# Kernel tuning notes

Measured on AMD Instinct MI355X. Metric: run time of the kernel, lower is better.

Reference implementation:

```python
import jax, jax.numpy as jnp
import numpy as np

NUMV = 779
B, NQ, NV = 1, 65536, 1558


def feat_sample(feat, xy):
    # feat [B,C,H,W], xy [B,N,2] in [-1,1]; bilinear, align_corners=True (grid_sample semantics)
    Bn, C, H, W = feat.shape
    x = (xy[..., 0] + 1.0) * 0.5 * (W - 1)
    y = (xy[..., 1] + 1.0) * 0.5 * (H - 1)
    x0f = jnp.floor(x); y0f = jnp.floor(y)
    wx = (x - x0f)[:, None, :]; wy = (y - y0f)[:, None, :]  # [B,1,N]
    x0 = jnp.clip(x0f, 0, W - 1).astype(jnp.int32)
    x1 = jnp.clip(x0f + 1, 0, W - 1).astype(jnp.int32)
    y0 = jnp.clip(y0f, 0, H - 1).astype(jnp.int32)
    y1 = jnp.clip(y0f + 1, 0, H - 1).astype(jnp.int32)
    g = jax.vmap(lambda f, yi, xi: f[:, yi, xi])  # [C,N] per batch
    v00 = g(feat, y0, x0); v01 = g(feat, y0, x1)
    v10 = g(feat, y1, x0); v11 = g(feat, y1, x1)
    out = v00 * (1 - wx) * (1 - wy) + v01 * wx * (1 - wy) + v10 * (1 - wx) * wy + v11 * wx * wy
    return jnp.transpose(out, (0, 2, 1))  # [B,N,C]


def conv2d(x, w):
    return jax.lax.conv_general_dilated(x, w, (1, 1), ((1, 1), (1, 1)), dimension_numbers=('NCHW', 'OIHW', 'NCHW'))


def conv1d3(x, w):
    return jax.lax.conv_general_dilated(x, w, (1,), ((1, 1),), dimension_numbers=('NCH', 'OIH', 'NCH'))


def ln(x, g, b):
    # LayerNorm over trailing dims matching g's shape, eps=1e-6
    axes = tuple(range(x.ndim - g.ndim, x.ndim))
    m = x.mean(axes, keepdims=True)
    v = x.var(axes, keepdims=True)
    return (x - m) / jnp.sqrt(v + 1e-6) * g + b


def apool3(x):
    # AdaptiveAvgPool2d(3), PyTorch window rule: [floor(i*L/3), ceil((i+1)*L/3))
    H, W = x.shape[-2], x.shape[-1]
    bnd = lambda L: [(int(np.floor(i * L / 3)), int(np.ceil((i + 1) * L / 3))) for i in range(3)]
    hb, wb = bnd(H), bnd(W)
    rows = []
    for (hs, he) in hb:
        rows.append(jnp.stack([x[:, :, hs:he, ws:we].mean((-2, -1)) for (ws, we) in wb], axis=-1))
    return jnp.stack(rows, axis=-2)  # [B,C,3,3]


def _forward(vert_xy, ft1, ft_xy, vert, v, vert_vis, query_vis, img_xy, img_fmap, latent_fused, fconv_w1, fconv_w2, at_w1, at_w2, gt_w1, gt_g1, gt_b1, gt_w2, gt_g2, gt_b2, c3_w1, c3_g1, c3_b1, c3_w2, c3_g2, c3_b2, c4_w1, c4_g1, c4_b1, c4_w2, c4_g2, c4_b2):
    Bn = vert_xy.shape[0]
    vf = jnp.concatenate([feat_sample(img_fmap, vert_xy), feat_sample(ft1, vert_xy)], axis=2)  # [B,NV,11]
    h = jax.nn.relu(ln(conv2d(ft1, c3_w1), c3_g1, c3_b1))
    h = jax.nn.relu(ln(conv2d(h, c3_w2), c3_g2, c3_b2))
    gf = apool3(h).reshape(Bn, 42, 9)
    h = jax.nn.relu(ln(conv2d(img_fmap, c4_w1), c4_g1, c4_b1))
    h = jax.nn.relu(ln(conv2d(h, c4_w2), c4_g2, c4_b2))
    gf_img = apool3(h).reshape(Bn, 42, 9)
    gf = jnp.concatenate([gf_img, gf], axis=-1)  # [B,42,18]
    h = jax.nn.relu(ln(conv1d3(gf, gt_w1), gt_g1, gt_b1))
    gf_vert = jax.nn.relu(ln(conv1d3(h, gt_w2), gt_g2, gt_b2))  # [B,1558,18]
    vf = jnp.concatenate([vf, gf_vert], axis=2)  # [B,1558,29]
    # KNN, K=1; indices taken from batch 0 exactly as the original does
    d2 = (v[0] ** 2).sum(-1)[:, None] + (vert[0] ** 2).sum(-1)[None, :] - 2.0 * jnp.einsum('qd,pd->qp', v[0], vert[0])  # [NQ,NV]
    idx = jnp.argmin(d2, axis=-1)  # [NQ]
    vf_toh = jnp.concatenate([vf[:, NUMV:], vf[:, :NUMV]], axis=1)
    vv_toh = jnp.concatenate([vert_vis[:, NUMV:], vert_vis[:, :NUMV]], axis=1)
    knn = vf[:, idx] * vert_vis[:, idx]        # [B,NQ,29]
    knn_toh = vf_toh[:, idx] * vv_toh[:, idx]
    vis_th = vert_vis[:, idx]                  # [B,NQ,1]
    vis_toh = vv_toh[:, idx]
    knn_gf, knn_f = knn[:, :, 11:], knn[:, :, :11]
    knn_toh_gf, knn_toh_f = knn_toh[:, :, 11:], knn_toh[:, :, :11]
    query_feat = jnp.concatenate([img_xy, ft_xy], axis=2)  # [B,NQ,11]
    y = jnp.concatenate([query_feat, knn_f, knn_toh_f, knn_gf, knn_toh_gf, latent_fused, query_vis, vis_th, vis_toh], axis=2)  # [B,NQ,96]
    at = jax.nn.sigmoid(jnp.einsum('oc,bnc->bno', at_w2, jax.nn.relu(jnp.einsum('oc,bnc->bno', at_w1, y))))  # [B,NQ,6]
    y2 = jnp.concatenate([query_feat * at[..., 0:1], knn_f * at[..., 1:2], knn_toh_f * at[..., 2:3], knn_gf * at[..., 3:4], knn_toh_gf * at[..., 4:5], latent_fused * at[..., 5:6], query_vis, vis_th, vis_toh], axis=2)  # [B,NQ,96]
    return jnp.einsum('oc,bnc->bno', fconv_w2, jax.nn.relu(jnp.einsum('oc,bnc->bno', fconv_w1, y2)))  # [B,NQ,40]


def setup_inputs():
    key = jax.random.key(0)
    ks = jax.random.split(key, 24)
    rn = lambda k, s, sc=1.0: jax.random.normal(k, s, dtype=jnp.float32) * sc
    return {
        'vert_xy': jax.random.uniform(ks[0], (B, NV, 2), minval=-1.0, maxval=1.0),
        'ft1': rn(ks[1], (B, 8, 64, 64)),
        'ft_xy': rn(ks[2], (B, NQ, 8)),
        'vert': rn(ks[3], (B, NV, 3)),
        'v': rn(ks[4], (B, NQ, 3)),
        'vert_vis': jax.random.uniform(ks[5], (B, NV, 1)),
        'query_vis': jax.random.uniform(ks[6], (B, NQ, 1)),
        'img_xy': rn(ks[7], (B, NQ, 3)),
        'img_fmap': rn(ks[8], (B, 3, 256, 256)),
        'latent_fused': rn(ks[9], (B, NQ, 24)),
        'fconv_w1': rn(ks[10], (96, 96), 0.1), 'fconv_w2': rn(ks[11], (40, 96), 0.1),
        'at_w1': rn(ks[12], (96, 96), 0.1), 'at_w2': rn(ks[13], (6, 96), 0.1),
        'gt_w1': rn(ks[14], (NUMV, 42, 3), 0.05), 'gt_g1': jnp.ones(18), 'gt_b1': jnp.zeros(18),
        'gt_w2': rn(ks[15], (2 * NUMV, NUMV, 3), 0.02), 'gt_g2': jnp.ones(18), 'gt_b2': jnp.zeros(18),
        'c3_w1': rn(ks[16], (21, 8, 3, 3), 0.1), 'c3_g1': jnp.ones((64, 64)), 'c3_b1': jnp.zeros((64, 64)),
        'c3_w2': rn(ks[17], (42, 21, 3, 3), 0.1), 'c3_g2': jnp.ones((64, 64)), 'c3_b2': jnp.zeros((64, 64)),
        'c4_w1': rn(ks[18], (21, 3, 3, 3), 0.1), 'c4_g1': jnp.ones((256, 256)), 'c4_b1': jnp.zeros((256, 256)),
        'c4_w2': rn(ks[19], (42, 21, 3, 3), 0.1), 'c4_g2': jnp.ones((256, 256)), 'c4_b2': jnp.zeros((256, 256)),
    }


def reference(vert_xy, ft1, ft_xy, vert, v, vert_vis, query_vis, img_xy, img_fmap, latent_fused, fconv_w1, fconv_w2, at_w1, at_w2, gt_w1, gt_g1, gt_b1, gt_w2, gt_g2, gt_b2, c3_w1, c3_g1, c3_b1, c3_w2, c3_g2, c3_b2, c4_w1, c4_g1, c4_b1, c4_w2, c4_g2, c4_b2):
    return _forward(vert_xy, ft1, ft_xy, vert, v, vert_vis, query_vis, img_xy, img_fmap, latent_fused, fconv_w1, fconv_w2, at_w1, at_w2, gt_w1, gt_g1, gt_b1, gt_w2, gt_g2, gt_b2, c3_w1, c3_g1, c3_b1, c3_w2, c3_g2, c3_b2, c4_w1, c4_g1, c4_b1, c4_w2, c4_g2, c4_b2)
```

## Files before the change

kernel.cpp:

```cpp
#include <hip/hip_runtime.h>
#include <hip/hip_bf16.h>
#include <math.h>

#define NQ_    65536
#define NV_    1558
#define HALF_V 779
#define VSPLIT 8
#define VCHUNK 195

#define WS_STATS 0
#define WS_GFC   512
#define WS_GTH   1280
#define WS_VF    15360
#define WS_C3A   65536
#define WS_C3B   151552
#define WS_C4A   323584
#define WS_C4B   1699840
#define WS_WBF   4452352
#define WS_PART  4464640
#define WS_IDX   4500480
#define WS_BESTD 4566016
#define WS_BESTI 5090304
#define WS_VERT4 5614592

typedef __attribute__((ext_vector_type(8))) short bf16x8;
typedef __attribute__((ext_vector_type(4))) float f32x4;

__device__ __forceinline__ short f2b(float x) {
    union { __hip_bfloat16 h; short s; } u; u.h = __float2bfloat16(x); return u.s;
}

__device__ __forceinline__ void bsample(const float* __restrict__ f, int C, int H, int W,
                                        float xn, float yn, float* __restrict__ o) {
    float x = (xn + 1.f) * 0.5f * (float)(W - 1);
    float y = (yn + 1.f) * 0.5f * (float)(H - 1);
    float x0f = floorf(x), y0f = floorf(y);
    float wx = x - x0f, wy = y - y0f;
    int x0 = (int)fminf(fmaxf(x0f, 0.f), (float)(W - 1));
    int x1 = (int)fminf(fmaxf(x0f + 1.f, 0.f), (float)(W - 1));
    int y0 = (int)fminf(fmaxf(y0f, 0.f), (float)(H - 1));
    int y1 = (int)fminf(fmaxf(y0f + 1.f, 0.f), (float)(H - 1));
    for (int c = 0; c < C; ++c) {
        const float* b = f + c * H * W;
        float v00 = b[y0 * W + x0], v01 = b[y0 * W + x1];
        float v10 = b[y1 * W + x0], v11 = b[y1 * W + x1];
        o[c] = v00 * (1.f - wx) * (1.f - wy) + v01 * wx * (1.f - wy)
             + v10 * (1.f - wx) * wy       + v11 * wx * wy;
    }
}

__device__ __forceinline__ void feat_body(int rb, int tid,
                                          const float* __restrict__ vert_xy,
                                          const float* __restrict__ img,
                                          const float* __restrict__ ft1,
                                          float* __restrict__ vf) {
    int v = rb * 256 + tid;
    if (v >= NV_) return;
    float xn = vert_xy[v * 2 + 0], yn = vert_xy[v * 2 + 1];
    float tmp[8];
    bsample(img, 3, 256, 256, xn, yn, tmp);
    float* o = vf + v * 32;
    o[0] = tmp[0]; o[1] = tmp[1]; o[2] = tmp[2];
    bsample(ft1, 8, 64, 64, xn, yn, tmp);
    #pragma unroll
    for (int c = 0; c < 8; ++c) o[3 + c] = tmp[c];
}

template <int CB>
__device__ __forceinline__ void conv_body(
    float* __restrict__ sm, int tid,
    const float* __restrict__ in, const float* __restrict__ w,
    float* __restrict__ out, float* __restrict__ part,
    int Cin, int H, int W, int bx, int by, int nbx) {
    int c0 = by * CB;
    int gpx0 = bx * 1024;
    int y0 = gpx0 / W;
    int tileF = 1024 + 2 * W;
    int nf4 = tileF >> 2;
    int HW = H * W;
    int px0 = tid * 4;
    int ty = px0 / W, x = px0 % W;

    float acc[CB][4];
    #pragma unroll
    for (int j = 0; j < CB; ++j)
        #pragma unroll
        for (int p = 0; p < 4; ++p) acc[j][p] = 0.f;

    const float* wbase = w + c0 * Cin * 9;
    float4 sreg[2];

    #pragma unroll
    for (int k = 0; k < 2; ++k) {
        int idx = tid + k * 256;
        float4 v = make_float4(0.f, 0.f, 0.f, 0.f);
        if (idx < nf4) {
            int gw = idx * 4;
            int gy = y0 - 1 + gw / W, gx = gw % W;
            if (gy >= 0 && gy < H) v = *(const float4*)(in + gy * W + gx);
        }
        sreg[k] = v;
    }
    #pragma unroll
    for (int k = 0; k < 2; ++k) {
        int idx = tid + k * 256;
        if (idx < nf4) *(float4*)(sm + 8 + idx * 4) = sreg[k];
    }
    __syncthreads();

    for (int ci = 0; ci < Cin; ++ci) {
        if (ci + 1 < Cin) {
            const float* ipn = in + (ci + 1) * HW;
            #pragma unroll
            for (int k = 0; k < 2; ++k) {
                int idx = tid + k * 256;
                float4 v = make_float4(0.f, 0.f, 0.f, 0.f);
                if (idx < nf4) {
                    int gw = idx * 4;
                    int gy = y0 - 1 + gw / W, gx = gw % W;
                    if (gy >= 0 && gy < H) v = *(const float4*)(ipn + gy * W + gx);
                }
                sreg[k] = v;
            }
        }
        {
            const float* tl = sm + (ci & 1) * 1552 + 8;
            float win[3][6];
            #pragma unroll
            for (int r = 0; r < 3; ++r) {
                const float* lrow = tl + (ty + r) * W + x;
                float4 B = *(const float4*)(lrow);
                float4 A = *(const float4*)(lrow - 4);
                float4 C = *(const float4*)(lrow + 4);
                win[r][0] = (x > 0) ? A.w : 0.f;
                win[r][1] = B.x; win[r][2] = B.y; win[r][3] = B.z; win[r][4] = B.w;
                win[r][5] = (x + 4 < W) ? C.x : 0.f;
            }
            const float* wc = wbase + ci * 9;
            #pragma unroll
            for (int j = 0; j < CB; ++j) {
                const float* wj = wc + j * Cin * 9;
                #pragma unroll
                for (int r = 0; r < 3; ++r) {
                    float w0 = wj[r * 3 + 0], w1 = wj[r * 3 + 1], w2 = wj[r * 3 + 2];
                    #pragma unroll
                    for (int p = 0; p < 4; ++p)
                        acc[j][p] = fmaf(w0, win[r][p],
                                    fmaf(w1, win[r][p + 1],
                                    fmaf(w2, win[r][p + 2], acc[j][p])));
                }
            }
        }
        if (ci + 1 < Cin) {
            float* tn = sm + ((ci + 1) & 1) * 1552 + 8;
            #pragma unroll
            for (int k = 0; k < 2; ++k) {
                int idx = tid + k * 256;
                if (idx < nf4) *(float4*)(tn + idx * 4) = sreg[k];
            }
        }
        __syncthreads();
    }

    #pragma unroll
    for (int j = 0; j < CB; ++j) {
        float4 o4 = make_float4(acc[j][0], acc[j][1], acc[j][2], acc[j][3]);
        *(float4*)(out + (c0 + j) * HW + gpx0 + px0) = o4;
    }

    float* sred = sm;
    int lane = tid & 63, wave = tid >> 6;
    #pragma unroll
    for (int j = 0; j < CB; ++j) {
        float s  = acc[j][0] + acc[j][1] + acc[j][2] + acc[j][3];
        float qq = acc[j][0] * acc[j][0] + acc[j][1] * acc[j][1]
                 + acc[j][2] * acc[j][2] + acc[j][3] * acc[j][3];
        #pragma unroll
        for (int off = 1; off < 64; off <<= 1) {
            s  += __shfl_xor(s, off, 64);
            qq += __shfl_xor(qq, off, 64);
        }
        if (lane == 0) { sred[(wave * CB + j) * 2 + 0] = s; sred[(wave * CB + j) * 2 + 1] = qq; }
    }
    __syncthreads();
    if (tid < CB) {
        float s = 0.f, qq = 0.f;
        #pragma unroll
        for (int wv = 0; wv < 4; ++wv) {
            s  += sred[(wv * CB + tid) * 2 + 0];
            qq += sred[(wv * CB + tid) * 2 + 1];
        }
        int c = c0 + tid;
        part[(c * nbx + bx) * 2 + 0] = s;
        part[(c * nbx + bx) * 2 + 1] = qq;
    }
}

__device__ __forceinline__ void wcvt_body(int rb, int tid,
    const float* __restrict__ atw1, const float* __restrict__ atw2,
    const float* __restrict__ fcw1, const float* __restrict__ fcw2,
    short* __restrict__ wb) {
    int i = rb * 256 + tid;
    short v = 0;
    if (i < 9216) v = f2b(atw1[i]);
    else if (i < 10752) { int j = i - 9216; v = (j < 576) ? f2b(atw2[j]) : (short)0; }
    else if (i < 19968) v = f2b(fcw1[i - 10752]);
    else { int j = i - 19968; v = (j < 3840) ? f2b(fcw2[j]) : (short)0; }
    wb[i] = v;
}

__device__ __forceinline__ void vprep_body(int rb, int tid,
    const float* __restrict__ vert, float4* __restrict__ v4) {
    int i = rb * 256 + tid;
    if (i >= NV_) return;
    float x = vert[i * 3 + 0], y = vert[i * 3 + 1], z = vert[i * 3 + 2];
    float pn = __fadd_rn(__fadd_rn(__fmul_rn(x, x), __fmul_rn(y, y)), __fmul_rn(z, z));
    v4[i] = make_float4(x, y, z, pn);
}

__device__ __forceinline__ void argmin_body(int qb, int r, int tid,
    const float* __restrict__ v, const float4* __restrict__ v4,
    float* __restrict__ bestd, int* __restrict__ besti) {
    int q = qb * 256 + tid;
    int p0 = r * VCHUNK;
    int p1 = p0 + VCHUNK; if (p1 > NV_) p1 = NV_;
    float vx = v[q * 3 + 0], vy = v[q * 3 + 1], vz = v[q * 3 + 2];
    float vn = __fadd_rn(__fadd_rn(__fmul_rn(vx, vx), __fmul_rn(vy, vy)), __fmul_rn(vz, vz));
    float best = 3.4e38f;
    int bi = p0;
    #pragma unroll 4
    for (int p = p0; p < p1; ++p) {
        float4 pv = v4[p];
        float dot = __fadd_rn(__fadd_rn(__fmul_rn(vx, pv.x), __fmul_rn(vy, pv.y)), __fmul_rn(vz, pv.z));
        float d2 = __fsub_rn(__fadd_rn(vn, pv.w), __fmul_rn(2.f, dot));
        if (d2 < best) { best = d2; bi = p; }
    }
    bestd[r * NQ_ + q] = best;
    besti[r * NQ_ + q] = bi;
}

__global__ __launch_bounds__(256) void megaA_k(
    const float* __restrict__ img, const float* __restrict__ c4w1,
    float* __restrict__ c4a, float* __restrict__ part_c4a,
    const float* __restrict__ ft1, const float* __restrict__ c3w1,
    float* __restrict__ c3a, float* __restrict__ part_c3a,
    const float* __restrict__ vert_xy, float* __restrict__ vfb,
    const float* __restrict__ atw1, const float* __restrict__ atw2,
    const float* __restrict__ fcw1, const float* __restrict__ fcw2,
    short* __restrict__ wbf,
    const float* __restrict__ vert, float4* __restrict__ vert4) {
    __shared__ float sm[2 * 1552];
    int rb = blockIdx.x, tid = threadIdx.x;
    if (rb < 192)       conv_body<7>(sm, tid, img, c4w1, c4a, part_c4a, 3, 256, 256, rb % 64, rb / 64, 64);
    else if (rb < 204)  { int r = rb - 192; conv_body<7>(sm, tid, ft1, c3w1, c3a, part_c3a, 8, 64, 64, r % 4, r / 4, 4); }
    else if (rb < 211)  feat_body(rb - 204, tid, vert_xy, img, ft1, vfb);
    else if (rb < 307)  wcvt_body(rb - 211, tid, atw1, atw2, fcw1, fcw2, wbf);
    else                vprep_body(rb - 307, tid, vert, vert4);
}

__global__ __launch_bounds__(256) void megaB_k(
    const float* __restrict__ c4a, const float* __restrict__ c4w2,
    float* __restrict__ c4bb, float* __restrict__ part_c4b,
    const float* __restrict__ c3a, const float* __restrict__ c3w2,
    float* __restrict__ c3bb, float* __restrict__ part_c3b,
    const float* __restrict__ v, const float4* __restrict__ vert4,
    float* __restrict__ bestd, int* __restrict__ besti) {
    __shared__ float sm[2 * 1552];
    int rb = blockIdx.x, tid = threadIdx.x;
    if (rb < 384)       conv_body<7>(sm, tid, c4a, c4w2, c4bb, part_c4b, 21, 256, 256, rb % 64, rb / 64, 64);
    else if (rb < 408)  { int r = rb - 384; conv_body<7>(sm, tid, c3a, c3w2, c3bb, part_c3b, 21, 64, 64, r % 4, r / 4, 4); }
    else                { int r = rb - 408; argmin_body(r % 256, r / 256, tid, v, vert4, bestd, besti); }
}

__device__ __forceinline__ void lnfin_body(int c, const float* __restrict__ part,
                                           float* __restrict__ stats, int C, int nb, float invHW) {
    if (c >= C) return;
    float s = 0.f, s2 = 0.f;
    for (int i = 0; i < nb; ++i) {
        s  += part[(c * nb + i) * 2 + 0];
        s2 += part[(c * nb + i) * 2 + 1];
    }
    float m = s * invHW;
    float var = s2 * invHW - m * m;
    if (var < 0.f) var = 0.f;
    stats[c * 2 + 0] = m;
    stats[c * 2 + 1] = rsqrtf(var + 1e-6f);
}

__global__ void lnfin2_k(const float* __restrict__ pa, float* __restrict__ sa, int Ca, int nba, float inva,
                         const float* __restrict__ pb, float* __restrict__ sb, int Cb, int nbb, float invb) {
    if (blockIdx.x == 0) lnfin_body(threadIdx.x, pa, sa, Ca, nba, inva);
    else                 lnfin_body(threadIdx.x, pb, sb, Cb, nbb, invb);
}

__global__ __launch_bounds__(256) void lnapply2_k(
    float* __restrict__ c4a, const float* __restrict__ st4,
    const float* __restrict__ g4, const float* __restrict__ b4,
    float* __restrict__ c3a, const float* __restrict__ st3,
    const float* __restrict__ g3, const float* __restrict__ b3) {
    int rb = blockIdx.x, tid = threadIdx.x;
    if (rb < 5376) {
        int i = rb * 256 + tid;
        int c = i >> 16, hw = i & 65535;
        float m = st4[c * 2], inv = st4[c * 2 + 1];
        float x = c4a[i];
        c4a[i] = fmaxf(fmaf((x - m) * inv, g4[hw], b4[hw]), 0.f);
    } else {
        int i = (rb - 5376) * 256 + tid;
        int c = i >> 12, hw = i & 4095;
        float m = st3[c * 2], inv = st3[c * 2 + 1];
        float x = c3a[i];
        c3a[i] = fmaxf(fmaf((x - m) * inv, g3[hw], b3[hw]), 0.f);
    }
}

__device__ __forceinline__ void apool_body(int rb, int tid, float* __restrict__ rs,
    const float* __restrict__ in, const float* __restrict__ stats,
    const float* __restrict__ g, const float* __restrict__ b,
    float* __restrict__ gfc, int H, int W, int colOff) {
    int c = rb / 9, bin = rb % 9;
    int bh = bin / 3, bw = bin % 3;
    int hs = bh * H / 3, he = ((bh + 1) * H + 2) / 3;
    int wsx = bw * W / 3, we = ((bw + 1) * W + 2) / 3;
    int rw = we - wsx, rh = he - hs, n = rw * rh;
    const float* bb = in + c * H * W;
    float m = stats[c * 2], inv = stats[c * 2 + 1];
    float s = 0.f;
    for (int t = tid; t < n; t += 256) {
        int iy = t / rw, ix = t % rw;
        int hw = (hs + iy) * W + (wsx + ix);
        float x = bb[hw];
        float r = fmaf((x - m) * inv, g[hw], b[hw]);
        s += fmaxf(r, 0.f);
    }
    rs[tid] = s;
    __syncthreads();
    for (int st = 128; st > 0; st >>= 1) {
        if (tid < st) rs[tid] += rs[tid + st];
        __syncthreads();
    }
    if (tid == 0) gfc[c * 18 + colOff + bin] = rs[0] / (float)n;
}

__global__ __launch_bounds__(256) void apoolcomb_k(
    const float* __restrict__ c4bb, const float* __restrict__ st4,
    const float* __restrict__ g4, const float* __restrict__ b4,
    const float* __restrict__ c3bb, const float* __restrict__ st3,
    const float* __restrict__ g3, const float* __restrict__ b3,
    float* __restrict__ gfc,
    const float* __restrict__ bestd, const int* __restrict__ besti,
    int* __restrict__ idx) {
    __shared__ float rs[256];
    int rb = blockIdx.x, tid = threadIdx.x;
    if (rb < 378)       apool_body(rb, tid, rs, c4bb, st4, g4, b4, gfc, 256, 256, 0);
    else if (rb < 756)  apool_body(rb - 378, tid, rs, c3bb, st3, g3, b3, gfc, 64, 64, 9);
    else {
        int q = (rb - 756) * 256 + tid;
        float best = bestd[q];
        int bi = besti[q];
        #pragma unroll
        for (int r = 1; r < VSPLIT; ++r) {
            float d = bestd[r * NQ_ + q];
            int i2 = besti[r * NQ_ + q];
            if (d < best) { best = d; bi = i2; }
        }
        idx[q] = bi;
    }
}

__global__ __launch_bounds__(64) void gt1_k(const float* __restrict__ gfc,
                                            const float* __restrict__ w,
                                            const float* __restrict__ g,
                                            const float* __restrict__ b,
                                            float* __restrict__ outh) {
    int o = blockIdx.x;
    int p = threadIdx.x;
    __shared__ float vals[18];
    if (p < 18) {
        float acc = 0.f;
        const float* wo = w + o * 42 * 3;
        for (int c = 0; c < 42; ++c) {
            const float* gr = gfc + c * 18;
            #pragma unroll
            for (int k = 0; k < 3; ++k) {
                int pk = p + k - 1;
                if (pk >= 0 && pk < 18) acc = fmaf(wo[c * 3 + k], gr[pk], acc);
            }
        }
        vals[p] = acc;
    }
    __syncthreads();
    if (p < 18) {
        float s = 0.f, s2 = 0.f;
        #pragma unroll
        for (int j = 0; j < 18; ++j) { float x = vals[j]; s += x; s2 += x * x; }
        float m = s / 18.f;
        float var = s2 / 18.f - m * m;
        if (var < 0.f) var = 0.f;
        float inv = rsqrtf(var + 1e-6f);
        float r = fmaf((vals[p] - m) * inv, g[p], b[p]);
        outh[o * 18 + p] = fmaxf(r, 0.f);
    }
}

__global__ __launch_bounds__(256) void gt2_k(const float* __restrict__ h,
                                             const float* __restrict__ w,
                                             const float* __restrict__ g,
                                             const float* __restrict__ b,
                                             float* __restrict__ vf) {
    int o = blockIdx.x;
    int t = threadIdx.x, lane = t & 63, wave = t >> 6;
    __shared__ float red[4][18];
    float part[18];
    #pragma unroll
    for (int p = 0; p < 18; ++p) part[p] = 0.f;
    int c0 = wave * 195;
    int c1 = c0 + 195; if (c1 > HALF_V) c1 = HALF_V;
    for (int c = c0 + lane; c < c1; c += 64) {
        const float* wr = w + (o * HALF_V + c) * 3;
        float w0 = wr[0], w1 = wr[1], w2 = wr[2];
        const float* hr = h + c * 18;
        float hv[18];
        #pragma unroll
        for (int p = 0; p < 18; ++p) hv[p] = hr[p];
        #pragma unroll
        for (int p = 0; p < 18; ++p) {
            float a = w1 * hv[p];
            if (p > 0)  a = fmaf(w0, hv[p - 1], a);
            if (p < 17) a = fmaf(w2, hv[p + 1], a);
            part[p] += a;
        }
    }
    #pragma unroll
    for (int p = 0; p < 18; ++p) {
        float vv = part[p];
        #pragma unroll
        for (int off = 32; off > 0; off >>= 1) vv += __shfl_xor(vv, off, 64);
        part[p] = vv;
    }
    if (lane == 0) {
        #pragma unroll
        for (int p = 0; p < 18; ++p) red[wave][p] = part[p];
    }
    __syncthreads();
    if (t < 18) {
        float s = red[0][t] + red[1][t] + red[2][t] + red[3][t];
        red[0][t] = s;
    }
    __syncthreads();
    if (t < 18) {
        float s = 0.f, s2 = 0.f;
        #pragma unroll
        for (int j = 0; j < 18; ++j) { float x = red[0][j]; s += x; s2 += x * x; }
        float m = s / 18.f;
        float var = s2 / 18.f - m * m;
        if (var < 0.f) var = 0.f;
        float inv = rsqrtf(var + 1e-6f);
        float r = fmaf((red[0][t] - m) * inv, g[t], b[t]);
        vf[o * 32 + 11 + t] = fmaxf(r, 0.f);
    }
}

#define YP 104

__global__ __launch_bounds__(256) void mlp_mfma_k(
    const int* __restrict__ idx,
    const float* __restrict__ vvis, const float* __restrict__ qvis,
    const float* __restrict__ ixy, const float* __restrict__ fxy,
    const float* __restrict__ lat, const float* __restrict__ vf,
    const short* __restrict__ wb, float* __restrict__ out) {
    __shared__ short Y[64 * YP];
    __shared__ short Hb[64 * YP];
    __shared__ float A6[64 * 8];
    int t = threadIdx.x;
    int lane = t & 63, wave = t >> 6;
    int q0 = blockIdx.x * 64;

    int ql = t >> 2, part = t & 3;
    int q = q0 + ql;
    int bi = idx[q];
    int bi2 = bi + HALF_V; if (bi2 >= NV_) bi2 -= NV_;
    const float* f  = vf + bi * 32;
    const float* ft = vf + bi2 * 32;
    float vis = vvis[bi], vist = vvis[bi2];
    short* yr = &Y[ql * YP];
    float myv[24];
    #pragma unroll
    for (int jj = 0; jj < 24; ++jj) {
        int j = part * 24 + jj;
        float val;
        if (j < 3)       val = ixy[q * 3 + j];
        else if (j < 11) val = fxy[q * 8 + j - 3];
        else if (j < 22) val = f[j - 11] * vis;
        else if (j < 33) val = ft[j - 22] * vist;
        else if (j < 51) val = f[11 + j - 33] * vis;
        else if (j < 69) val = ft[11 + j - 51] * vist;
        else if (j < 93) val = lat[q * 24 + j - 69];
        else if (j == 93) val = qvis[q];
        else if (j == 94) val = vis;
        else              val = vist;
        myv[jj] = val;
        yr[j] = f2b(val);
    }
    __syncthreads();

    int nloc = lane & 15, quad = lane >> 4;
    const short* Ya = &Y[(wave * 16 + nloc) * YP];
    const short* Ha = &Hb[(wave * 16 + nloc) * YP];
    int hrow = wave * 16 + quad * 4;

    f32x4 acc[6];
    #pragma unroll
    for (int nt = 0; nt < 6; ++nt) acc[nt] = (f32x4){0.f, 0.f, 0.f, 0.f};
    #pragma unroll
    for (int k0 = 0; k0 < 96; k0 += 32) {
        bf16x8 a = *(const bf16x8*)(Ya + k0 + quad * 8);
        #pragma unroll
        for (int nt = 0; nt < 6; ++nt) {
            bf16x8 b = *(const bf16x8*)(wb + (nt * 16 + nloc) * 96 + k0 + quad * 8);
            acc[nt] = __builtin_amdgcn_mfma_f32_16x16x32_bf16(a, b, acc[nt], 0, 0, 0);
        }
    }
    #pragma unroll
    for (int nt = 0; nt < 6; ++nt)
        #pragma unroll
        for (int r = 0; r < 4; ++r)
            Hb[(hrow + r) * YP + nt * 16 + nloc] = f2b(fmaxf(acc[nt][r], 0.f));
    __syncthreads();

    {
        const short* w2 = wb + 9216;
        f32x4 a2 = (f32x4){0.f, 0.f, 0.f, 0.f};
        #pragma unroll
        for (int k0 = 0; k0 < 96; k0 += 32) {
            bf16x8 a = *(const bf16x8*)(Ha + k0 + quad * 8);
            bf16x8 b = *(const bf16x8*)(w2 + nloc * 96 + k0 + quad * 8);
            a2 = __builtin_amdgcn_mfma_f32_16x16x32_bf16(a, b, a2, 0, 0, 0);
        }
        if (nloc < 6) {
            #pragma unroll
            for (int r = 0; r < 4; ++r)
                A6[(hrow + r) * 8 + nloc] = 1.f / (1.f + expf(-a2[r]));
        }
    }
    __syncthreads();

    {
        const float* ap = &A6[ql * 8];
        #pragma unroll
        for (int jj = 0; jj < 24; ++jj) {
            int j = part * 24 + jj;
            float s;
            if (j < 11)      s = ap[0];
            else if (j < 22) s = ap[1];
            else if (j < 33) s = ap[2];
            else if (j < 51) s = ap[3];
            else if (j < 69) s = ap[4];
            else if (j < 93) s = ap[5];
            else             s = 1.f;
            yr[j] = f2b(myv[jj] * s);
        }
    }
    __syncthreads();

    {
        const short* w3 = wb + 10752;
        #pragma unroll
        for (int nt = 0; nt < 6; ++nt) acc[nt] = (f32x4){0.f, 0.f, 0.f, 0.f};
        #pragma unroll
        for (int k0 = 0; k0 < 96; k0 += 32) {
            bf16x8 a = *(const bf16x8*)(Ya + k0 + quad * 8);
            #pragma unroll
            for (int nt = 0; nt < 6; ++nt) {
                bf16x8 b = *(const bf16x8*)(w3 + (nt * 16 + nloc) * 96 + k0 + quad * 8);
                acc[nt] = __builtin_amdgcn_mfma_f32_16x16x32_bf16(a, b, acc[nt], 0, 0, 0);
            }
        }
        #pragma unroll
        for (int nt = 0; nt < 6; ++nt)
            #pragma unroll
            for (int r = 0; r < 4; ++r)
                Hb[(hrow + r) * YP + nt * 16 + nloc] = f2b(fmaxf(acc[nt][r], 0.f));
    }
    __syncthreads();

    {
        const short* w4 = wb + 19968;
        f32x4 oacc[3];
        #pragma unroll
        for (int nt = 0; nt < 3; ++nt) oacc[nt] = (f32x4){0.f, 0.f, 0.f, 0.f};
        #pragma unroll
        for (int k0 = 0; k0 < 96; k0 += 32) {
            bf16x8 a = *(const bf16x8*)(Ha + k0 + quad * 8);
            #pragma unroll
            for (int nt = 0; nt < 3; ++nt) {
                bf16x8 b = *(const bf16x8*)(w4 + (nt * 16 + nloc) * 96 + k0 + quad * 8);
                oacc[nt] = __builtin_amdgcn_mfma_f32_16x16x32_bf16(a, b, oacc[nt], 0, 0, 0);
            }
        }
        #pragma unroll
        for (int nt = 0; nt < 3; ++nt) {
            int oc = nt * 16 + nloc;
            if (oc < 40) {
                #pragma unroll
                for (int r = 0; r < 4; ++r)
                    out[(q0 + hrow + r) * 40 + oc] = oacc[nt][r];
            }
        }
    }
}

extern "C" void kernel_launch(void* const* d_in, const int* in_sizes, int n_in,
                              void* d_out, int out_size, void* d_ws, size_t ws_size,
                              hipStream_t stream) {
    const float* vert_xy = (const float*)d_in[0];
    const float* ft1     = (const float*)d_in[1];
    const float* ft_xy   = (const float*)d_in[2];
    const float* vert    = (const float*)d_in[3];
    const float* v       = (const float*)d_in[4];
    const float* vvis    = (const float*)d_in[5];
    const float* qvis    = (const float*)d_in[6];
    const float* ixy     = (const float*)d_in[7];
    const float* img     = (const float*)d_in[8];
    const float* lat     = (const float*)d_in[9];
    const float* fcw1    = (const float*)d_in[10];
    const float* fcw2    = (const float*)d_in[11];
    const float* atw1    = (const float*)d_in[12];
    const float* atw2    = (const float*)d_in[13];
    const float* gtw1    = (const float*)d_in[14];
    const float* gtg1    = (const float*)d_in[15];
    const float* gtb1    = (const float*)d_in[16];
    const float* gtw2    = (const float*)d_in[17];
    const float* gtg2    = (const float*)d_in[18];
    const float* gtb2    = (const float*)d_in[19];
    const float* c3w1    = (const float*)d_in[20];
    const float* c3g1    = (const float*)d_in[21];
    const float* c3b1    = (const float*)d_in[22];
    const float* c3w2    = (const float*)d_in[23];
    const float* c3g2    = (const float*)d_in[24];
    const float* c3b2    = (const float*)d_in[25];
    const float* c4w1    = (const float*)d_in[26];
    const float* c4g1    = (const float*)d_in[27];
    const float* c4b1    = (const float*)d_in[28];
    const float* c4w2    = (const float*)d_in[29];
    const float* c4g2    = (const float*)d_in[30];
    const float* c4b2    = (const float*)d_in[31];
    float* out = (float*)d_out;
    float* ws  = (float*)d_ws;
    float* stats = ws + WS_STATS;
    float* gfc   = ws + WS_GFC;
    float* gth   = ws + WS_GTH;
    float* vfb   = ws + WS_VF;
    float* c3a   = ws + WS_C3A;
    float* c3bb  = ws + WS_C3B;
    float* c4a   = ws + WS_C4A;
    float* c4bb  = ws + WS_C4B;
    short* wbf   = (short*)(ws + WS_WBF);
    float* part_c3a = ws + WS_PART + 0;
    float* part_c4a = ws + WS_PART + 8192;
    float* part_c3b = ws + WS_PART + 16384;
    float* part_c4b = ws + WS_PART + 24576;
    int*    idx   = (int*)(ws + WS_IDX);
    float*  bestd = ws + WS_BESTD;
    int*    besti = (int*)(ws + WS_BESTI);
    float4* vert4 = (float4*)(ws + WS_VERT4);

    megaA_k<<<314, 256, 0, stream>>>(img, c4w1, c4a, part_c4a,
                                     ft1, c3w1, c3a, part_c3a,
                                     vert_xy, vfb,
                                     atw1, atw2, fcw1, fcw2, wbf,
                                     vert, vert4);
    lnfin2_k<<<2, 64, 0, stream>>>(part_c3a, stats + 0, 21, 4, 1.f / 4096.f,
                                   part_c4a, stats + 256, 21, 64, 1.f / 65536.f);
    lnapply2_k<<<5712, 256, 0, stream>>>(c4a, stats + 256, c4g1, c4b1,
                                         c3a, stats + 0, c3g1, c3b1);
    megaB_k<<<2456, 256, 0, stream>>>(c4a, c4w2, c4bb, part_c4b,
                                      c3a, c3w2, c3bb, part_c3b,
                                      v, vert4, bestd, besti);
    lnfin2_k<<<2, 64, 0, stream>>>(part_c3b, stats + 128, 42, 4, 1.f / 4096.f,
                                   part_c4b, stats + 384, 42, 64, 1.f / 65536.f);
    apoolcomb_k<<<1012, 256, 0, stream>>>(c4bb, stats + 384, c4g2, c4b2,
                                          c3bb, stats + 128, c3g2, c3b2,
                                          gfc, bestd, besti, idx);
    gt1_k<<<779, 64, 0, stream>>>(gfc, gtw1, gtg1, gtb1, gth);
    gt2_k<<<1558, 256, 0, stream>>>(gth, gtw2, gtg2, gtb2, vfb);
    mlp_mfma_k<<<NQ_ / 64, 256, 0, stream>>>(idx, vvis, qvis, ixy, ft_xy, lat, vfb,
                                             wbf, out);
}
```

Measured before the change: 286.5 us.

## Move nearest-vertex argmin into first megakernel with LDS-staged vertices

The brute-force nearest-vertex search moves from the second fused kernel into the first. Each block now computes its chunk of vertex positions and squared norms into shared memory, which removes the separate vertex-prep pass and its global buffer. The cross-chunk argmin reduction moves from the pooling kernel into the second fused kernel. This rebalances work so the search overlaps with the first, smaller conv stage, but it makes that stage's grid much larger and adds a block barrier.

```diff
diff --git a/kernel.cpp b/kernel.cpp
--- a/kernel.cpp
+++ b/kernel.cpp
@@ -21,7 +21,6 @@
 #define WS_IDX   4500480
 #define WS_BESTD 4566016
 #define WS_BESTI 5090304
-#define WS_VERT4 5614592
 
 typedef __attribute__((ext_vector_type(8))) short bf16x8;
 typedef __attribute__((ext_vector_type(4))) float f32x4;
@@ -209,31 +208,30 @@
     wb[i] = v;
 }
 
-__device__ __forceinline__ void vprep_body(int rb, int tid,
-    const float* __restrict__ vert, float4* __restrict__ v4) {
-    int i = rb * 256 + tid;
-    if (i >= NV_) return;
-    float x = vert[i * 3 + 0], y = vert[i * 3 + 1], z = vert[i * 3 + 2];
-    float pn = __fadd_rn(__fadd_rn(__fmul_rn(x, x), __fmul_rn(y, y)), __fmul_rn(z, z));
-    v4[i] = make_float4(x, y, z, pn);
-}
-
-__device__ __forceinline__ void argmin_body(int qb, int r, int tid,
-    const float* __restrict__ v, const float4* __restrict__ v4,
+__device__ __forceinline__ void argmin_body(int qb, int r, int tid, float4* __restrict__ sv,
+    const float* __restrict__ v, const float* __restrict__ vert,
     float* __restrict__ bestd, int* __restrict__ besti) {
-    int q = qb * 256 + tid;
     int p0 = r * VCHUNK;
     int p1 = p0 + VCHUNK; if (p1 > NV_) p1 = NV_;
+    int n = p1 - p0;
+    if (tid < n) {
+        int p = p0 + tid;
+        float x = vert[p * 3 + 0], y = vert[p * 3 + 1], z = vert[p * 3 + 2];
+        float pn = __fadd_rn(__fadd_rn(__fmul_rn(x, x), __fmul_rn(y, y)), __fmul_rn(z, z));
+        sv[tid] = make_float4(x, y, z, pn);
+    }
+    __syncthreads();
+    int q = qb * 256 + tid;
     float vx = v[q * 3 + 0], vy = v[q * 3 + 1], vz = v[q * 3 + 2];
     float vn = __fadd_rn(__fadd_rn(__fmul_rn(vx, vx), __fmul_rn(vy, vy)), __fmul_rn(vz, vz));
     float best = 3.4e38f;
     int bi = p0;
     #pragma unroll 4
-    for (int p = p0; p < p1; ++p) {
-        float4 pv = v4[p];
+    for (int i = 0; i < n; ++i) {
+        float4 pv = sv[i];
         float dot = __fadd_rn(__fadd_rn(__fmul_rn(vx, pv.x), __fmul_rn(vy, pv.y)), __fmul_rn(vz, pv.z));
         float d2 = __fsub_rn(__fadd_rn(vn, pv.w), __fmul_rn(2.f, dot));
-        if (d2 < best) { best = d2; bi = p; }
+        if (d2 < best) { best = d2; bi = p0 + i; }
     }
     bestd[r * NQ_ + q] = best;
     besti[r * NQ_ + q] = bi;
@@ -248,14 +246,15 @@
     const float* __restrict__ atw1, const float* __restrict__ atw2,
     const float* __restrict__ fcw1, const float* __restrict__ fcw2,
     short* __restrict__ wbf,
-    const float* __restrict__ vert, float4* __restrict__ vert4) {
-    __shared__ float sm[2 * 1552];
+    const float* __restrict__ v, const float* __restrict__ vert,
+    float* __restrict__ bestd, int* __restrict__ besti) {
+    __shared__ __align__(16) float sm[2 * 1552];
     int rb = blockIdx.x, tid = threadIdx.x;
     if (rb < 192)       conv_body<7>(sm, tid, img, c4w1, c4a, part_c4a, 3, 256, 256, rb % 64, rb / 64, 64);
     else if (rb < 204)  { int r = rb - 192; conv_body<7>(sm, tid, ft1, c3w1, c3a, part_c3a, 8, 64, 64, r % 4, r / 4, 4); }
-    else if (rb < 211)  feat_body(rb - 204, tid, vert_xy, img, ft1, vfb);
-    else if (rb < 307)  wcvt_body(rb - 211, tid, atw1, atw2, fcw1, fcw2, wbf);
-    else                vprep_body(rb - 307, tid, vert, vert4);
+    else if (rb < 2252) { int r = rb - 204; argmin_body(r % 256, r / 256, tid, (float4*)sm, v, vert, bestd, besti); }
+    else if (rb < 2259) feat_body(rb - 2252, tid, vert_xy, img, ft1, vfb);
+    else                wcvt_body(rb - 2259, tid, atw1, atw2, fcw1, fcw2, wbf);
 }
 
 __global__ __launch_bounds__(256) void megaB_k(
@@ -263,13 +262,24 @@
     float* __restrict__ c4bb, float* __restrict__ part_c4b,
     const float* __restrict__ c3a, const float* __restrict__ c3w2,
     float* __restrict__ c3bb, float* __restrict__ part_c3b,
-    const float* __restrict__ v, const float4* __restrict__ vert4,
-    float* __restrict__ bestd, int* __restrict__ besti) {
-    __shared__ float sm[2 * 1552];
+    const float* __restrict__ bestd, const int* __restrict__ besti,
+    int* __restrict__ idx) {
+    __shared__ __align__(16) float sm[2 * 1552];
     int rb = blockIdx.x, tid = threadIdx.x;
     if (rb < 384)       conv_body<7>(sm, tid, c4a, c4w2, c4bb, part_c4b, 21, 256, 256, rb % 64, rb / 64, 64);
     else if (rb < 408)  { int r = rb - 384; conv_body<7>(sm, tid, c3a, c3w2, c3bb, part_c3b, 21, 64, 64, r % 4, r / 4, 4); }
-    else                { int r = rb - 408; argmin_body(r % 256, r / 256, tid, v, vert4, bestd, besti); }
+    else {
+        int q = (rb - 408) * 256 + tid;
+        float best = bestd[q];
+        int bi = besti[q];
+        #pragma unroll
+        for (int r = 1; r < VSPLIT; ++r) {
+            float d = bestd[r * NQ_ + q];
+            int i2 = besti[r * NQ_ + q];
+            if (d < best) { best = d; bi = i2; }
+        }
+        idx[q] = bi;
+    }
 }
 
 __device__ __forceinline__ void lnfin_body(int c, const float* __restrict__ part,
@@ -342,30 +352,16 @@
     if (tid == 0) gfc[c * 18 + colOff + bin] = rs[0] / (float)n;
 }
 
-__global__ __launch_bounds__(256) void apoolcomb_k(
+__global__ __launch_bounds__(256) void apool2_k(
     const float* __restrict__ c4bb, const float* __restrict__ st4,
     const float* __restrict__ g4, const float* __restrict__ b4,
     const float* __restrict__ c3bb, const float* __restrict__ st3,
     const float* __restrict__ g3, const float* __restrict__ b3,
-    float* __restrict__ gfc,
-    const float* __restrict__ bestd, const int* __restrict__ besti,
-    int* __restrict__ idx) {
+    float* __restrict__ gfc) {
     __shared__ float rs[256];
     int rb = blockIdx.x, tid = threadIdx.x;
-    if (rb < 378)       apool_body(rb, tid, rs, c4bb, st4, g4, b4, gfc, 256, 256, 0);
-    else if (rb < 756)  apool_body(rb - 378, tid, rs, c3bb, st3, g3, b3, gfc, 64, 64, 9);
-    else {
-        int q = (rb - 756) * 256 + tid;
-        float best = bestd[q];
-        int bi = besti[q];
-        #pragma unroll
-        for (int r = 1; r < VSPLIT; ++r) {
-            float d = bestd[r * NQ_ + q];
-            int i2 = besti[r * NQ_ + q];
-            if (d < best) { best = d; bi = i2; }
-        }
-        idx[q] = bi;
-    }
+    if (rb < 378) apool_body(rb, tid, rs, c4bb, st4, g4, b4, gfc, 256, 256, 0);
+    else          apool_body(rb - 378, tid, rs, c3bb, st3, g3, b3, gfc, 64, 64, 9);
 }
 
 __global__ __launch_bounds__(64) void gt1_k(const float* __restrict__ gfc,
@@ -663,25 +659,23 @@
     int*    idx   = (int*)(ws + WS_IDX);
     float*  bestd = ws + WS_BESTD;
     int*    besti = (int*)(ws + WS_BESTI);
-    float4* vert4 = (float4*)(ws + WS_VERT4);
-
-    megaA_k<<<314, 256, 0, stream>>>(img, c4w1, c4a, part_c4a,
-                                     ft1, c3w1, c3a, part_c3a,
-                                     vert_xy, vfb,
-                                     atw1, atw2, fcw1, fcw2, wbf,
-                                     vert, vert4);
+
+    megaA_k<<<2355, 256, 0, stream>>>(img, c4w1, c4a, part_c4a,
+                                      ft1, c3w1, c3a, part_c3a,
+                                      vert_xy, vfb,
+                                      atw1, atw2, fcw1, fcw2, wbf,
+                                      v, vert, bestd, besti);
     lnfin2_k<<<2, 64, 0, stream>>>(part_c3a, stats + 0, 21, 4, 1.f / 4096.f,
                                    part_c4a, stats + 256, 21, 64, 1.f / 65536.f);
     lnapply2_k<<<5712, 256, 0, stream>>>(c4a, stats + 256, c4g1, c4b1,
                                          c3a, stats + 0, c3g1, c3b1);
-    megaB_k<<<2456, 256, 0, stream>>>(c4a, c4w2, c4bb, part_c4b,
-                                      c3a, c3w2, c3bb, part_c3b,
-                                      v, vert4, bestd, besti);
+    megaB_k<<<664, 256, 0, stream>>>(c4a, c4w2, c4bb, part_c4b,
+                                     c3a, c3w2, c3bb, part_c3b,
+                                     bestd, besti, idx);
     lnfin2_k<<<2, 64, 0, stream>>>(part_c3b, stats + 128, 42, 4, 1.f / 4096.f,
                                    part_c4b, stats + 384, 42, 64, 1.f / 65536.f);
-    apoolcomb_k<<<1012, 256, 0, stream>>>(c4bb, stats + 384, c4g2, c4b2,
-                                          c3bb, stats + 128, c3g2, c3b2,
-                                          gfc, bestd, besti, idx);
+    apool2_k<<<756, 256, 0, stream>>>(c4bb, stats + 384, c4g2, c4b2,
+                                      c3bb, stats + 128, c3g2, c3b2, gfc);
     gt1_k<<<779, 64, 0, stream>>>(gfc, gtw1, gtg1, gtb1, gth);
     gt2_k<<<1558, 256, 0, stream>>>(gth, gtw2, gtg2, gtb2, vfb);
     mlp_mfma_k<<<NQ_ / 64, 256, 0, stream>>>(idx, vvis, qvis, ixy, ft_xy, lat, vfb,
```

After: 288.2 us. No clear change (+0.6%).
